# Performance work log

Hardware: AMD Instinct MI355X
Metric: run time of the kernel (lower is better)

The kernel has to match this reference:

```python
import jax, jax.numpy as jnp
import numpy as np

B, N, F = 4096, 128, 3
EPS = 1e-5


def _bn(x, g, b):
    # BatchNorm1d(element_num) on [B, N, C]: channels are dim 1 (the N elements);
    # training-mode stats over dims (0, 2), biased variance (torch default).
    m = x.mean(axis=(0, 2), keepdims=True)
    v = ((x - m) ** 2).mean(axis=(0, 2), keepdims=True)
    return (x - m) / jnp.sqrt(v + EPS) * g[None, :, None] + b[None, :, None]


def _rel(x, W, bvec, psi, phi, wr):
    # f'_i = wr/N * sum_{j != i} (psi*phi * <x_i, x_j>) * relu(unary(x_j))
    n = x.shape[1]
    U = jax.nn.relu(jnp.einsum('bnd,ed->bne', x, W) + bvec)       # [B,N,D]
    S = (psi * phi) * jnp.einsum('bnd,bmd->bnm', x, x)            # [B,N,N]
    S = S * (1.0 - jnp.eye(n, dtype=x.dtype))                     # exclude j == i
    return wr * jnp.einsum('bnm,bmd->bnd', S, U) / n


def setup_inputs() -> dict:
    key = jax.random.key(0)
    ks = iter(jax.random.split(key, 64))
    d1, d2 = 2 * F, 4 * F  # 6, 12

    def w(shape, s=0.1):
        return (jax.random.normal(next(ks), shape, dtype=jnp.float32) * s)

    def scalar():
        return jax.random.uniform(next(ks), (), dtype=jnp.float32)

    inp = {
        'x': jax.random.normal(next(ks), (B, N, F), dtype=jnp.float32),
        'fc1_w': w((d1, F)), 'fc1_b': w((d1,)),
        'bn1_g': jnp.ones((N,), jnp.float32), 'bn1_b': jnp.zeros((N,), jnp.float32),
        'fc2_w': w((d2, d1)), 'fc2_b': w((d2,)),
        'bn2_g': jnp.ones((N,), jnp.float32), 'bn2_b': jnp.zeros((N,), jnp.float32),
        'fc3_w': w((d2, d2)), 'fc3_b': w((d2,)),
        'u1_w': w((d2, d2)), 'u1_b': w((d2,)), 'ps1': scalar(), 'ph1': scalar(), 'wr1': scalar(),
        'u2_w': w((d2, d2)), 'u2_b': w((d2,)), 'ps2': scalar(), 'ph2': scalar(), 'wr2': scalar(),
        'u3_w': w((d2, d2)), 'u3_b': w((d2,)), 'ps3': scalar(), 'ph3': scalar(), 'wr3': scalar(),
        'u4_w': w((d2, d2)), 'u4_b': w((d2,)), 'ps4': scalar(), 'ph4': scalar(), 'wr4': scalar(),
        'fc4_w': w((d1, d2)), 'fc4_b': w((d1,)),
        'bn4_g': jnp.ones((N,), jnp.float32), 'bn4_b': jnp.zeros((N,), jnp.float32),
        'fc5_w': w((F, d1)), 'fc5_b': w((F,)),
        'fc6_w': w((1, F)), 'fc6_b': w((1,)),
        'fc7_w': w((F - 1, F)), 'fc7_b': w((F - 1,)),
        'fc8_w': w((1, F)), 'fc8_b': w((1,)),
    }
    return inp


def reference(x, fc1_w, fc1_b, bn1_g, bn1_b, fc2_w, fc2_b, bn2_g, bn2_b,
              fc3_w, fc3_b,
              u1_w, u1_b, ps1, ph1, wr1,
              u2_w, u2_b, ps2, ph2, wr2,
              u3_w, u3_b, ps3, ph3, wr3,
              u4_w, u4_b, ps4, ph4, wr4,
              fc4_w, fc4_b, bn4_g, bn4_b,
              fc5_w, fc5_b, fc6_w, fc6_b, fc7_w, fc7_b, fc8_w, fc8_b):
    h = jax.nn.relu(_bn(jnp.einsum('bnf,ef->bne', x, fc1_w) + fc1_b, bn1_g, bn1_b))
    h = jax.nn.relu(_bn(jnp.einsum('bnf,ef->bne', h, fc2_w) + fc2_b, bn2_g, bn2_b))
    h = jax.nn.sigmoid(jnp.einsum('bnf,ef->bne', h, fc3_w) + fc3_b)
    h = _rel(h, u1_w, u1_b, ps1, ph1, wr1)
    h = _rel(h, u2_w, u2_b, ps2, ph2, wr2)
    h = _rel(h, u3_w, u3_b, ps3, ph3, wr3)
    h = _rel(h, u4_w, u4_b, ps4, ph4, wr4)
    h = jax.nn.relu(_bn(jnp.einsum('bnf,ef->bne', h, fc4_w) + fc4_b, bn4_g, bn4_b))
    h = jax.nn.relu(jnp.einsum('bnf,ef->bne', h, fc5_w) + fc5_b)
    cls = jnp.einsum('bnf,ef->bne', h, fc6_w) + fc6_b          # [B,N,1]
    geo = jnp.einsum('bnf,ef->bne', h, fc7_w) + fc7_b          # [B,N,F-1]
    res = jnp.concatenate([cls, geo], axis=2)                   # [B,N,F]
    pres = res.max(axis=1)                                      # MaxPool1d over all N -> [B,F]
    pred = jax.nn.sigmoid(pres @ fc8_w.T + fc8_b)               # [B,1]
    return pred
```

## Files before the change

kernel.cpp:

```cpp
#include <hip/hip_runtime.h>
#include <hip/hip_fp16.h>

#define BB 4096
#define NN 128
#define EPS 1e-5f

#define S1 0
#define S2 2048
#define S4 4096
#define A4_OFF 6144

static __device__ __forceinline__ float sigmoidf_(float z){
  return 1.f/(1.f+__expf(-z));
}
static __device__ __forceinline__ float2 h2f2_(unsigned u){
  __half2 h = *reinterpret_cast<__half2*>(&u);
  return __half22float2(h);
}

static __device__ __forceinline__ float fdot2_(unsigned a, unsigned b, float c){
#if defined(__has_builtin)
#if __has_builtin(__builtin_amdgcn_fdot2)
  typedef _Float16 h2v __attribute__((ext_vector_type(2)));
  h2v av = *reinterpret_cast<h2v*>(&a);
  h2v bv = *reinterpret_cast<h2v*>(&b);
  return __builtin_amdgcn_fdot2(av, bv, c, false);
#else
  float2 af = h2f2_(a), bf = h2f2_(b);
  return fmaf(af.y, bf.y, fmaf(af.x, bf.x, c));
#endif
#else
  float2 af = h2f2_(a), bf = h2f2_(b);
  return fmaf(af.y, bf.y, fmaf(af.x, bf.x, c));
#endif
}

__global__ __launch_bounds__(256) void k1(const float* __restrict__ x, const float* __restrict__ w1,
                   const float* __restrict__ b1, float* __restrict__ st){
  __shared__ float bl[512];
  const int t = threadIdx.x;
  const int tid = blockIdx.x*256 + t;
  float W[18], Bv[6];
  #pragma unroll
  for (int i=0;i<18;i++) W[i]=w1[i];
  #pragma unroll
  for (int i=0;i<6;i++) Bv[i]=b1[i];
  float s=0.f, sq=0.f;
  #pragma unroll
  for (int kk=0;kk<2;kk++){
    const int r = tid + kk*262144;
    const float* xr = x + (size_t)r*3;
    float x0=xr[0], x1=xr[1], x2=xr[2];
    #pragma unroll
    for (int e=0;e<6;e++){
      float a = fmaf(x0,W[e*3+0], fmaf(x1,W[e*3+1], fmaf(x2,W[e*3+2], Bv[e])));
      s+=a; sq=fmaf(a,a,sq);
    }
  }
  bl[t]=s; bl[256+t]=sq;
  __syncthreads();
  const int shadow = (blockIdx.x & 7)*256;
  if (t<128) atomicAdd(&st[S1+shadow+t], bl[t]+bl[t+128]);
  else       atomicAdd(&st[S1+shadow+t], bl[t+128]+bl[t+256]);
}

__global__ __launch_bounds__(256) void k2(const float* __restrict__ x,
                   const float* __restrict__ w1, const float* __restrict__ b1,
                   const float* __restrict__ g1, const float* __restrict__ bb1,
                   const float* __restrict__ w2, const float* __restrict__ b2,
                   float* __restrict__ st){
  __shared__ float bl[512];
  const int t = threadIdx.x;
  const int tid = blockIdx.x*256 + t;
  const int n = t & 127;
  float ss=0.f, qs=0.f;
  #pragma unroll
  for (int c=0;c<8;c++){ ss+=st[S1+c*256+n]; qs+=st[S1+c*256+128+n]; }
  const float mean = ss*(1.f/(BB*6));
  const float var  = qs*(1.f/(BB*6)) - mean*mean;
  const float sc = g1[n]*rsqrtf(var+EPS), sh = bb1[n]-mean*sc;
  float W1[18], B1v[6], W2[72], B2v[12];
  #pragma unroll
  for (int i=0;i<18;i++) W1[i]=w1[i];
  #pragma unroll
  for (int i=0;i<6;i++) B1v[i]=b1[i];
  #pragma unroll
  for (int i=0;i<72;i++) W2[i]=w2[i];
  #pragma unroll
  for (int i=0;i<12;i++) B2v[i]=b2[i];
  float s=0.f, sq=0.f;
  #pragma unroll
  for (int kk=0;kk<2;kk++){
    const int r = tid + kk*262144;
    const float* xr = x + (size_t)r*3;
    float x0=xr[0], x1=xr[1], x2=xr[2];
    float h[6];
    #pragma unroll
    for (int e=0;e<6;e++){
      float a = fmaf(x0,W1[e*3+0], fmaf(x1,W1[e*3+1], fmaf(x2,W1[e*3+2], B1v[e])));
      h[e]=fmaxf(fmaf(a,sc,sh),0.f);
    }
    #pragma unroll
    for (int d=0;d<12;d++){
      float z=B2v[d];
      #pragma unroll
      for (int e=0;e<6;e++) z=fmaf(h[e],W2[d*6+e],z);
      s+=z; sq=fmaf(z,z,sq);
    }
  }
  bl[t]=s; bl[256+t]=sq;
  __syncthreads();
  const int shadow = (blockIdx.x & 7)*256;
  if (t<128) atomicAdd(&st[S2+shadow+t], bl[t]+bl[t+128]);
  else       atomicAdd(&st[S2+shadow+t], bl[t+128]+bl[t+256]);
}

__global__ __launch_bounds__(256) void k3(
  const float* __restrict__ x,
  const float* __restrict__ w1, const float* __restrict__ b1,
  const float* __restrict__ g1, const float* __restrict__ bb1,
  const float* __restrict__ w2, const float* __restrict__ b2,
  const float* __restrict__ g2, const float* __restrict__ bb2,
  const float* __restrict__ w3, const float* __restrict__ b3,
  const float* __restrict__ u1w, const float* __restrict__ u1b,
  const float* __restrict__ ps1, const float* __restrict__ ph1, const float* __restrict__ wr1,
  const float* __restrict__ u2w, const float* __restrict__ u2b,
  const float* __restrict__ ps2, const float* __restrict__ ph2, const float* __restrict__ wr2,
  const float* __restrict__ u3w, const float* __restrict__ u3b,
  const float* __restrict__ ps3, const float* __restrict__ ph3, const float* __restrict__ wr3,
  const float* __restrict__ u4w, const float* __restrict__ u4b,
  const float* __restrict__ ps4, const float* __restrict__ ph4, const float* __restrict__ wr4,
  const float* __restrict__ w4, const float* __restrict__ b4,
  __half* __restrict__ a4, float* __restrict__ st)
{
  __shared__ float lds[4][1536];
  const int wave = threadIdx.x >> 6;
  const int lane = threadIdx.x & 63;
  const int b = blockIdx.x*4 + wave;
  unsigned* Xp = (unsigned*)&lds[wave][0];
  unsigned* Up = (unsigned*)&lds[wave][768];
  const int r0 = lane*2, r1 = r0+1;

  float s1a=0,q1a=0,s1b=0,q1b=0,s2a=0,q2a=0,s2b=0,q2b=0;
  #pragma unroll
  for (int c=0;c<8;c++){
    s1a+=st[S1+c*256+r0]; q1a+=st[S1+c*256+128+r0];
    s1b+=st[S1+c*256+r1]; q1b+=st[S1+c*256+128+r1];
    s2a+=st[S2+c*256+r0]; q2a+=st[S2+c*256+128+r0];
    s2b+=st[S2+c*256+r1]; q2b+=st[S2+c*256+128+r1];
  }
  const float inv1 = 1.f/(BB*6), inv2 = 1.f/(BB*12);
  float m = s1a*inv1, v = q1a*inv1 - m*m;
  const float sA0 = g1[r0]*rsqrtf(v+EPS), hA0 = bb1[r0]-m*sA0;
  m = s1b*inv1; v = q1b*inv1 - m*m;
  const float sA1 = g1[r1]*rsqrtf(v+EPS), hA1 = bb1[r1]-m*sA1;
  m = s2a*inv2; v = q2a*inv2 - m*m;
  const float sB0 = g2[r0]*rsqrtf(v+EPS), hB0 = bb2[r0]-m*sB0;
  m = s2b*inv2; v = q2b*inv2 - m*m;
  const float sB1 = g2[r1]*rsqrtf(v+EPS), hB1 = bb2[r1]-m*sB1;

  const float2* xr = (const float2*)(x + ((size_t)b*128 + r0)*3);
  float2 c0=xr[0], c1=xr[1], c2=xr[2];
  const float xa0=c0.x, xa1=c0.y, xa2=c1.x;
  const float xb0=c1.y, xb1=c2.x, xb2=c2.y;

  float X0[12], X1[12];
  {
    float g6a[6], g6b[6];
    #pragma unroll
    for (int e=0;e<6;e++){
      float a0 = fmaf(xa0,w1[e*3+0], fmaf(xa1,w1[e*3+1], fmaf(xa2,w1[e*3+2], b1[e])));
      float a1v= fmaf(xb0,w1[e*3+0], fmaf(xb1,w1[e*3+1], fmaf(xb2,w1[e*3+2], b1[e])));
      g6a[e]=fmaxf(fmaf(a0,sA0,hA0),0.f);
      g6b[e]=fmaxf(fmaf(a1v,sA1,hA1),0.f);
    }
    float h0[12], h1[12];
    #pragma unroll
    for (int d=0;d<12;d++){
      float z0=b2[d], z1=b2[d];
      #pragma unroll
      for (int e=0;e<6;e++){ z0=fmaf(g6a[e],w2[d*6+e],z0); z1=fmaf(g6b[e],w2[d*6+e],z1); }
      h0[d]=fmaxf(fmaf(z0,sB0,hB0),0.f);
      h1[d]=fmaxf(fmaf(z1,sB1,hB1),0.f);
    }
    #pragma unroll
    for (int d=0; d<12; d++){
      float z0=b3[d], z1=b3[d];
      #pragma unroll
      for (int e=0;e<12;e++){ z0=fmaf(h0[e],w3[d*12+e],z0); z1=fmaf(h1[e],w3[d*12+e],z1); }
      X0[d]=sigmoidf_(z0); X1[d]=sigmoidf_(z1);
    }
  }

  const float* UW[4]  = {u1w,u2w,u3w,u4w};
  const float* UBv[4] = {u1b,u2b,u3b,u4b};
  const float cf[4] = {
    wr1[0]*ps1[0]*ph1[0]*(1.f/128.f),
    wr2[0]*ps2[0]*ph2[0]*(1.f/128.f),
    wr3[0]*ps3[0]*ph3[0]*(1.f/128.f),
    wr4[0]*ps4[0]*ph4[0]*(1.f/128.f)
  };

  const int g = lane>>4;
  int kc = lane & 15; if (kc>11) kc=11;

  #pragma unroll
  for (int l=0;l<4;l++){
    const float* uw = UW[l];
    const float* ub = UBv[l];
    const float coef = cf[l];
    float Y0[12], Y1[12];
    {
      float U0[12], U1[12];
      #pragma unroll
      for (int d=0;d<12;d++){
        float z0=ub[d], z1=ub[d];
        #pragma unroll
        for (int e=0;e<12;e++){ z0=fmaf(X0[e],uw[d*12+e],z0); z1=fmaf(X1[e],uw[d*12+e],z1); }
        U0[d]=fmaxf(z0,0.f); U1[d]=fmaxf(z1,0.f);
      }
      float q0=0.f, q1=0.f;
      #pragma unroll
      for (int e=0;e<12;e++){ q0=fmaf(X0[e],X0[e],q0); q1=fmaf(X1[e],X1[e],q1); }
      __half2 hp[12], up[12];
      #pragma unroll
      for (int e=0;e<12;e++){
        hp[e] = __floats2half2_rn(X0[e],X1[e]);
        up[e] = __floats2half2_rn(U0[e],U1[e]);
      }
      {
        const uint4* hpv = (const uint4*)hp;
        const uint4* upv = (const uint4*)up;
        uint4* xw = (uint4*)(Xp + lane*12);
        uint4* uwp = (uint4*)(Up + lane*12);
        xw[0]=hpv[0]; xw[1]=hpv[1]; xw[2]=hpv[2];
        uwp[0]=upv[0]; uwp[1]=upv[1]; uwp[2]=upv[2];
      }
      const float q0c = coef*q0, q1c = coef*q1;
      #pragma unroll
      for (int d=0;d<12;d++){ Y0[d] = -q0c*U0[d]; Y1[d] = -q1c*U1[d]; }
    }

    float mp[12];
    #pragma unroll
    for (int d=0;d<12;d++) mp[d]=0.f;
    #pragma unroll
    for (int i=0;i<16;i++){
      const int p = (g<<4) | ((i+g)&15);
      const unsigned xv2 = Xp[p*12 + kc];
      const uint4* urow = (const uint4*)(Up + p*12);
      uint4 ua=urow[0], ub4=urow[1], uc=urow[2];
      mp[0]=fdot2_(xv2, ua.x, mp[0]);  mp[1]=fdot2_(xv2, ua.y, mp[1]);
      mp[2]=fdot2_(xv2, ua.z, mp[2]);  mp[3]=fdot2_(xv2, ua.w, mp[3]);
      mp[4]=fdot2_(xv2, ub4.x, mp[4]); mp[5]=fdot2_(xv2, ub4.y, mp[5]);
      mp[6]=fdot2_(xv2, ub4.z, mp[6]); mp[7]=fdot2_(xv2, ub4.w, mp[7]);
      mp[8]=fdot2_(xv2, uc.x, mp[8]);  mp[9]=fdot2_(xv2, uc.y, mp[9]);
      mp[10]=fdot2_(xv2, uc.z, mp[10]); mp[11]=fdot2_(xv2, uc.w, mp[11]);
    }
    #pragma unroll
    for (int d=0;d<12;d++) mp[d] += __shfl_xor(mp[d], 16, 64);
    #pragma unroll
    for (int d=0;d<12;d++) mp[d] += __shfl_xor(mp[d], 32, 64);
    #pragma unroll
    for (int d=0;d<12;d++) mp[d] *= coef;

    #pragma unroll
    for (int k=0;k<12;k++){
      const float xa = X0[k], xb = X1[k];
      #pragma unroll
      for (int d=0;d<12;d++){
        const float mv = __int_as_float(__builtin_amdgcn_readlane(__float_as_int(mp[d]), k));
        Y0[d]=fmaf(xa,mv,Y0[d]); Y1[d]=fmaf(xb,mv,Y1[d]);
      }
    }
    #pragma unroll
    for (int d=0;d<12;d++){ X0[d]=Y0[d]; X1[d]=Y1[d]; }
  }

  float z0[6], z1[6];
  float s0=0.f,sq0=0.f,s1=0.f,sq1=0.f;
  #pragma unroll
  for (int e=0;e<6;e++){
    float a0=b4[e], a1v=b4[e];
    #pragma unroll
    for (int d=0;d<12;d++){ a0=fmaf(X0[d],w4[e*12+d],a0); a1v=fmaf(X1[d],w4[e*12+d],a1v); }
    z0[e]=a0; z1[e]=a1v;
    s0+=a0; sq0=fmaf(a0,a0,sq0); s1+=a1v; sq1=fmaf(a1v,a1v,sq1);
  }
  {
    __half2 ha[6];
    ha[0]=__floats2half2_rn(z0[0],z0[1]); ha[1]=__floats2half2_rn(z0[2],z0[3]); ha[2]=__floats2half2_rn(z0[4],z0[5]);
    ha[3]=__floats2half2_rn(z1[0],z1[1]); ha[4]=__floats2half2_rn(z1[2],z1[3]); ha[5]=__floats2half2_rn(z1[4],z1[5]);
    const uint2* hv = (const uint2*)ha;
    uint2* aw = (uint2*)(a4 + ((size_t)b*128 + r0)*6);
    aw[0]=hv[0]; aw[1]=hv[1]; aw[2]=hv[2];
  }

  __syncthreads();
  lds[wave][r0]=s0; lds[wave][r1]=s1;
  lds[wave][128+r0]=sq0; lds[wave][128+r1]=sq1;
  __syncthreads();
  const int t = threadIdx.x;
  const int c = (blockIdx.x & 7)*256;
  atomicAdd(&st[S4 + c + t], lds[0][t]+lds[1][t]+lds[2][t]+lds[3][t]);
}

__global__ __launch_bounds__(256) void k4(
  const __half* __restrict__ a4, const float* __restrict__ g4, const float* __restrict__ bb4,
  const float* __restrict__ w5, const float* __restrict__ b5,
  const float* __restrict__ w6, const float* __restrict__ b6,
  const float* __restrict__ w7, const float* __restrict__ b7,
  const float* __restrict__ w8, const float* __restrict__ b8,
  const float* __restrict__ st, float* __restrict__ out)
{
  const int wave = threadIdx.x>>6, lane = threadIdx.x&63;
  const int b = blockIdx.x*4 + wave;
  const int r0 = lane*2, r1 = r0+1;
  float ss0=0.f, qq0=0.f, ss1=0.f, qq1=0.f;
  #pragma unroll
  for (int cc=0;cc<8;cc++){
    ss0 += st[S4+cc*256+r0];     qq0 += st[S4+cc*256+128+r0];
    ss1 += st[S4+cc*256+r1];     qq1 += st[S4+cc*256+128+r1];
  }
  const float inv = 1.f/(BB*6);
  const float mean0 = ss0*inv, var0 = qq0*inv - mean0*mean0;
  const float sc0 = g4[r0]*rsqrtf(var0+EPS), sh0 = bb4[r0]-mean0*sc0;
  const float mean1 = ss1*inv, var1 = qq1*inv - mean1*mean1;
  const float sc1 = g4[r1]*rsqrtf(var1+EPS), sh1 = bb4[r1]-mean1*sc1;

  const uint2* ar = (const uint2*)(a4 + ((size_t)b*128 + r0)*6);
  uint2 v0=ar[0], v1=ar[1], v2=ar[2];
  float2 f0=h2f2_(v0.x), f1=h2f2_(v0.y), f2=h2f2_(v1.x);
  float2 f3=h2f2_(v1.y), f4=h2f2_(v2.x), f5=h2f2_(v2.y);
  float h0[6] = {f0.x,f0.y,f1.x,f1.y,f2.x,f2.y};
  float h1[6] = {f3.x,f3.y,f4.x,f4.y,f5.x,f5.y};
  #pragma unroll
  for (int e=0;e<6;e++){
    h0[e]=fmaxf(fmaf(h0[e],sc0,sh0),0.f);
    h1[e]=fmaxf(fmaf(h1[e],sc1,sh1),0.f);
  }
  float mx[3];
  {
    float h5a[3], h5b[3];
    #pragma unroll
    for (int f=0;f<3;f++){
      float za=b5[f], zb=b5[f];
      #pragma unroll
      for (int e=0;e<6;e++){ za=fmaf(h0[e],w5[f*6+e],za); zb=fmaf(h1[e],w5[f*6+e],zb); }
      h5a[f]=fmaxf(za,0.f); h5b[f]=fmaxf(zb,0.f);
    }
    float ca=b6[0], cb=b6[0];
    float g0a=b7[0], g0b=b7[0], g1a=b7[1], g1b=b7[1];
    #pragma unroll
    for (int f=0;f<3;f++){
      ca=fmaf(h5a[f],w6[f],ca);   cb=fmaf(h5b[f],w6[f],cb);
      g0a=fmaf(h5a[f],w7[f],g0a); g0b=fmaf(h5b[f],w7[f],g0b);
      g1a=fmaf(h5a[f],w7[3+f],g1a); g1b=fmaf(h5b[f],w7[3+f],g1b);
    }
    mx[0]=fmaxf(ca,cb); mx[1]=fmaxf(g0a,g0b); mx[2]=fmaxf(g1a,g1b);
  }
  #pragma unroll
  for (int off=32; off>0; off>>=1){
    mx[0]=fmaxf(mx[0], __shfl_xor(mx[0],off,64));
    mx[1]=fmaxf(mx[1], __shfl_xor(mx[1],off,64));
    mx[2]=fmaxf(mx[2], __shfl_xor(mx[2],off,64));
  }
  if (lane==0){
    float z = b8[0] + mx[0]*w8[0] + mx[1]*w8[1] + mx[2]*w8[2];
    out[b]=sigmoidf_(z);
  }
}

extern "C" void kernel_launch(void* const* d_in, const int* in_sizes, int n_in,
                              void* d_out, int out_size, void* d_ws, size_t ws_size,
                              hipStream_t stream){
  const float* x   = (const float*)d_in[0];
  const float* f1w = (const float*)d_in[1];
  const float* f1b = (const float*)d_in[2];
  const float* g1  = (const float*)d_in[3];
  const float* bb1 = (const float*)d_in[4];
  const float* f2w = (const float*)d_in[5];
  const float* f2b = (const float*)d_in[6];
  const float* g2  = (const float*)d_in[7];
  const float* bb2 = (const float*)d_in[8];
  const float* f3w = (const float*)d_in[9];
  const float* f3b = (const float*)d_in[10];
  const float* u1w = (const float*)d_in[11];
  const float* u1b = (const float*)d_in[12];
  const float* ps1 = (const float*)d_in[13];
  const float* ph1 = (const float*)d_in[14];
  const float* wr1 = (const float*)d_in[15];
  const float* u2w = (const float*)d_in[16];
  const float* u2b = (const float*)d_in[17];
  const float* ps2 = (const float*)d_in[18];
  const float* ph2 = (const float*)d_in[19];
  const float* wr2 = (const float*)d_in[20];
  const float* u3w = (const float*)d_in[21];
  const float* u3b = (const float*)d_in[22];
  const float* ps3 = (const float*)d_in[23];
  const float* ph3 = (const float*)d_in[24];
  const float* wr3 = (const float*)d_in[25];
  const float* u4w = (const float*)d_in[26];
  const float* u4b = (const float*)d_in[27];
  const float* ps4 = (const float*)d_in[28];
  const float* ph4 = (const float*)d_in[29];
  const float* wr4 = (const float*)d_in[30];
  const float* f4w = (const float*)d_in[31];
  const float* f4b = (const float*)d_in[32];
  const float* g4  = (const float*)d_in[33];
  const float* bb4 = (const float*)d_in[34];
  const float* f5w = (const float*)d_in[35];
  const float* f5b = (const float*)d_in[36];
  const float* f6w = (const float*)d_in[37];
  const float* f6b = (const float*)d_in[38];
  const float* f7w = (const float*)d_in[39];
  const float* f7b = (const float*)d_in[40];
  const float* f8w = (const float*)d_in[41];
  const float* f8b = (const float*)d_in[42];

  float* wsf = (float*)d_ws;
  float* st  = wsf;
  __half* a4 = (__half*)(wsf + A4_OFF);
  float* out = (float*)d_out;

  k1<<<dim3(1024), dim3(256), 0, stream>>>(x, f1w, f1b, st);
  k2<<<dim3(1024), dim3(256), 0, stream>>>(x, f1w, f1b, g1, bb1, f2w, f2b, st);
  k3<<<dim3(1024), dim3(256), 0, stream>>>(x, f1w, f1b, g1, bb1, f2w, f2b, g2, bb2,
      f3w, f3b,
      u1w,u1b,ps1,ph1,wr1, u2w,u2b,ps2,ph2,wr2,
      u3w,u3b,ps3,ph3,wr3, u4w,u4b,ps4,ph4,wr4,
      f4w, f4b, a4, st);
  k4<<<dim3(1024), dim3(256), 0, stream>>>(a4, g4, bb4, f5w, f5b,
      f6w, f6b, f7w, f7b, f8w, f8b, st, out);
}
```

Measured before the change: 199.9 us.

## Fuse four kernels into one persistent kernel with grid barriers between BatchNorm stages

Replaces the four separate launches with a single kernel that keeps per-row activations in registers across the BatchNorm statistic phases and uses a hierarchical atomic grid barrier to wait for the global sums. This removes recomputation of the early layers, the fp16 round-trip of the fc4 activations through global memory, and the launch gaps between kernels. It also switches arithmetic to two-wide float vectors for packed FMA. The design relies on all 1024 blocks being co-resident (launch bounds 256,4), adds a memset launch, and has a spin guard that could silently proceed if residency is not met.

```diff
diff --git a/kernel.cpp b/kernel.cpp
--- a/kernel.cpp
+++ b/kernel.cpp
@@ -8,7 +8,7 @@
 #define S1 0
 #define S2 2048
 #define S4 4096
-#define A4_OFF 6144
+#define BAR_OFF 6144
 
 static __device__ __forceinline__ float sigmoidf_(float z){
   return 1.f/(1.f+__expf(-z));
@@ -16,6 +16,35 @@
 static __device__ __forceinline__ float2 h2f2_(unsigned u){
   __half2 h = *reinterpret_cast<__half2*>(&u);
   return __half22float2(h);
+}
+
+typedef float v2f __attribute__((ext_vector_type(2)));
+static __device__ __forceinline__ v2f vfma(v2f a, v2f b, v2f c){
+#if defined(__has_builtin)
+#if __has_builtin(__builtin_elementwise_fma)
+  return __builtin_elementwise_fma(a,b,c);
+#else
+  v2f r; r.x=fmaf(a.x,b.x,c.x); r.y=fmaf(a.y,b.y,c.y); return r;
+#endif
+#else
+  v2f r; r.x=fmaf(a.x,b.x,c.x); r.y=fmaf(a.y,b.y,c.y); return r;
+#endif
+}
+static __device__ __forceinline__ v2f vfmas(v2f a, float s, v2f c){
+  v2f b = {s,s};
+  return vfma(a,b,c);
+}
+static __device__ __forceinline__ v2f vmax0(v2f a){
+#if defined(__has_builtin)
+#if __has_builtin(__builtin_elementwise_max)
+  v2f z = {0.f,0.f};
+  return __builtin_elementwise_max(a,z);
+#else
+  v2f r; r.x=fmaxf(a.x,0.f); r.y=fmaxf(a.y,0.f); return r;
+#endif
+#else
+  v2f r; r.x=fmaxf(a.x,0.f); r.y=fmaxf(a.y,0.f); return r;
+#endif
 }
 
 static __device__ __forceinline__ float fdot2_(unsigned a, unsigned b, float c){
@@ -35,87 +64,32 @@
 #endif
 }
 
-__global__ __launch_bounds__(256) void k1(const float* __restrict__ x, const float* __restrict__ w1,
-                   const float* __restrict__ b1, float* __restrict__ st){
-  __shared__ float bl[512];
-  const int t = threadIdx.x;
-  const int tid = blockIdx.x*256 + t;
-  float W[18], Bv[6];
-  #pragma unroll
-  for (int i=0;i<18;i++) W[i]=w1[i];
-  #pragma unroll
-  for (int i=0;i<6;i++) Bv[i]=b1[i];
-  float s=0.f, sq=0.f;
-  #pragma unroll
-  for (int kk=0;kk<2;kk++){
-    const int r = tid + kk*262144;
-    const float* xr = x + (size_t)r*3;
-    float x0=xr[0], x1=xr[1], x2=xr[2];
-    #pragma unroll
-    for (int e=0;e<6;e++){
-      float a = fmaf(x0,W[e*3+0], fmaf(x1,W[e*3+1], fmaf(x2,W[e*3+2], Bv[e])));
-      s+=a; sq=fmaf(a,a,sq);
-    }
-  }
-  bl[t]=s; bl[256+t]=sq;
+static __device__ __forceinline__ float cload_f(const float* p){
+  return __hip_atomic_load(p, __ATOMIC_RELAXED, __HIP_MEMORY_SCOPE_AGENT);
+}
+static __device__ __forceinline__ int cload_i(const int* p){
+  return __hip_atomic_load(p, __ATOMIC_RELAXED, __HIP_MEMORY_SCOPE_AGENT);
+}
+
+static __device__ __forceinline__ void gbar(int* __restrict__ bar, int phase){
   __syncthreads();
-  const int shadow = (blockIdx.x & 7)*256;
-  if (t<128) atomicAdd(&st[S1+shadow+t], bl[t]+bl[t+128]);
-  else       atomicAdd(&st[S1+shadow+t], bl[t+128]+bl[t+256]);
-}
-
-__global__ __launch_bounds__(256) void k2(const float* __restrict__ x,
-                   const float* __restrict__ w1, const float* __restrict__ b1,
-                   const float* __restrict__ g1, const float* __restrict__ bb1,
-                   const float* __restrict__ w2, const float* __restrict__ b2,
-                   float* __restrict__ st){
-  __shared__ float bl[512];
-  const int t = threadIdx.x;
-  const int tid = blockIdx.x*256 + t;
-  const int n = t & 127;
-  float ss=0.f, qs=0.f;
-  #pragma unroll
-  for (int c=0;c<8;c++){ ss+=st[S1+c*256+n]; qs+=st[S1+c*256+128+n]; }
-  const float mean = ss*(1.f/(BB*6));
-  const float var  = qs*(1.f/(BB*6)) - mean*mean;
-  const float sc = g1[n]*rsqrtf(var+EPS), sh = bb1[n]-mean*sc;
-  float W1[18], B1v[6], W2[72], B2v[12];
-  #pragma unroll
-  for (int i=0;i<18;i++) W1[i]=w1[i];
-  #pragma unroll
-  for (int i=0;i<6;i++) B1v[i]=b1[i];
-  #pragma unroll
-  for (int i=0;i<72;i++) W2[i]=w2[i];
-  #pragma unroll
-  for (int i=0;i<12;i++) B2v[i]=b2[i];
-  float s=0.f, sq=0.f;
-  #pragma unroll
-  for (int kk=0;kk<2;kk++){
-    const int r = tid + kk*262144;
-    const float* xr = x + (size_t)r*3;
-    float x0=xr[0], x1=xr[1], x2=xr[2];
-    float h[6];
-    #pragma unroll
-    for (int e=0;e<6;e++){
-      float a = fmaf(x0,W1[e*3+0], fmaf(x1,W1[e*3+1], fmaf(x2,W1[e*3+2], B1v[e])));
-      h[e]=fmaxf(fmaf(a,sc,sh),0.f);
-    }
-    #pragma unroll
-    for (int d=0;d<12;d++){
-      float z=B2v[d];
-      #pragma unroll
-      for (int e=0;e<6;e++) z=fmaf(h[e],W2[d*6+e],z);
-      s+=z; sq=fmaf(z,z,sq);
-    }
-  }
-  bl[t]=s; bl[256+t]=sq;
+  if (threadIdx.x == 0){
+    int* base = bar + phase*2048;
+    int* grp  = base + (blockIdx.x & 63)*16;
+    int* root = base + 1024;
+    int old = __hip_atomic_fetch_add(grp, 1, __ATOMIC_RELAXED, __HIP_MEMORY_SCOPE_AGENT);
+    if (old == 15)
+      __hip_atomic_fetch_add(root, 1, __ATOMIC_RELAXED, __HIP_MEMORY_SCOPE_AGENT);
+    int guard = 0;
+    while (cload_i(root) < 64 && guard < (1<<22)){
+      __builtin_amdgcn_s_sleep(1);
+      ++guard;
+    }
+  }
   __syncthreads();
-  const int shadow = (blockIdx.x & 7)*256;
-  if (t<128) atomicAdd(&st[S2+shadow+t], bl[t]+bl[t+128]);
-  else       atomicAdd(&st[S2+shadow+t], bl[t+128]+bl[t+256]);
-}
-
-__global__ __launch_bounds__(256) void k3(
+}
+
+__global__ __launch_bounds__(256, 4) void kf(
   const float* __restrict__ x,
   const float* __restrict__ w1, const float* __restrict__ b1,
   const float* __restrict__ g1, const float* __restrict__ bb1,
@@ -131,64 +105,107 @@
   const float* __restrict__ u4w, const float* __restrict__ u4b,
   const float* __restrict__ ps4, const float* __restrict__ ph4, const float* __restrict__ wr4,
   const float* __restrict__ w4, const float* __restrict__ b4,
-  __half* __restrict__ a4, float* __restrict__ st)
+  const float* __restrict__ g4, const float* __restrict__ bb4,
+  const float* __restrict__ w5, const float* __restrict__ b5,
+  const float* __restrict__ w6, const float* __restrict__ b6,
+  const float* __restrict__ w7, const float* __restrict__ b7,
+  const float* __restrict__ w8, const float* __restrict__ b8,
+  float* __restrict__ st, int* __restrict__ bar, float* __restrict__ out)
 {
   __shared__ float lds[4][1536];
-  const int wave = threadIdx.x >> 6;
-  const int lane = threadIdx.x & 63;
+  __shared__ float stg[256];
+  const int t = threadIdx.x;
+  const int wave = t >> 6, lane = t & 63;
   const int b = blockIdx.x*4 + wave;
+  const int r0 = lane*2, r1 = r0+1;
+  const int shadow = (blockIdx.x & 7)*256;
   unsigned* Xp = (unsigned*)&lds[wave][0];
   unsigned* Up = (unsigned*)&lds[wave][768];
-  const int r0 = lane*2, r1 = r0+1;
-
-  float s1a=0,q1a=0,s1b=0,q1b=0,s2a=0,q2a=0,s2b=0,q2b=0;
-  #pragma unroll
-  for (int c=0;c<8;c++){
-    s1a+=st[S1+c*256+r0]; q1a+=st[S1+c*256+128+r0];
-    s1b+=st[S1+c*256+r1]; q1b+=st[S1+c*256+128+r1];
-    s2a+=st[S2+c*256+r0]; q2a+=st[S2+c*256+128+r0];
-    s2b+=st[S2+c*256+r1]; q2b+=st[S2+c*256+128+r1];
-  }
-  const float inv1 = 1.f/(BB*6), inv2 = 1.f/(BB*12);
-  float m = s1a*inv1, v = q1a*inv1 - m*m;
-  const float sA0 = g1[r0]*rsqrtf(v+EPS), hA0 = bb1[r0]-m*sA0;
-  m = s1b*inv1; v = q1b*inv1 - m*m;
-  const float sA1 = g1[r1]*rsqrtf(v+EPS), hA1 = bb1[r1]-m*sA1;
-  m = s2a*inv2; v = q2a*inv2 - m*m;
-  const float sB0 = g2[r0]*rsqrtf(v+EPS), hB0 = bb2[r0]-m*sB0;
-  m = s2b*inv2; v = q2b*inv2 - m*m;
-  const float sB1 = g2[r1]*rsqrtf(v+EPS), hB1 = bb2[r1]-m*sB1;
 
   const float2* xr = (const float2*)(x + ((size_t)b*128 + r0)*3);
   float2 c0=xr[0], c1=xr[1], c2=xr[2];
-  const float xa0=c0.x, xa1=c0.y, xa2=c1.x;
-  const float xb0=c1.y, xb1=c2.x, xb2=c2.y;
-
-  float X0[12], X1[12];
+  const v2f xx0 = {c0.x, c1.y};
+  const v2f xx1 = {c0.y, c2.x};
+  const v2f xx2 = {c1.x, c2.y};
+
+  v2f a6[6];
   {
-    float g6a[6], g6b[6];
+    v2f s={0.f,0.f}, q={0.f,0.f};
     #pragma unroll
     for (int e=0;e<6;e++){
-      float a0 = fmaf(xa0,w1[e*3+0], fmaf(xa1,w1[e*3+1], fmaf(xa2,w1[e*3+2], b1[e])));
-      float a1v= fmaf(xb0,w1[e*3+0], fmaf(xb1,w1[e*3+1], fmaf(xb2,w1[e*3+2], b1[e])));
-      g6a[e]=fmaxf(fmaf(a0,sA0,hA0),0.f);
-      g6b[e]=fmaxf(fmaf(a1v,sA1,hA1),0.f);
-    }
-    float h0[12], h1[12];
+      v2f v = {b1[e], b1[e]};
+      v = vfmas(xx2, w1[e*3+2], v);
+      v = vfmas(xx1, w1[e*3+1], v);
+      v = vfmas(xx0, w1[e*3+0], v);
+      a6[e]=v;
+      s += v; q = vfma(v,v,q);
+    }
+    lds[wave][r0]=s.x; lds[wave][r1]=s.y;
+    lds[wave][128+r0]=q.x; lds[wave][128+r1]=q.y;
+    __syncthreads();
+    atomicAdd(&st[S1 + shadow + t], lds[0][t]+lds[1][t]+lds[2][t]+lds[3][t]);
+  }
+  gbar(bar, 0);
+
+  v2f zv[12];
+  {
+    float acc=0.f;
+    #pragma unroll
+    for (int c=0;c<8;c++) acc += cload_f(&st[S1 + c*256 + t]);
+    stg[t]=acc;
+    __syncthreads();
+    const float inv1 = 1.f/(BB*6);
+    float m=stg[r0]*inv1, v=stg[128+r0]*inv1-m*m;
+    const float sA0=g1[r0]*rsqrtf(v+EPS), hA0=bb1[r0]-m*sA0;
+    m=stg[r1]*inv1; v=stg[128+r1]*inv1-m*m;
+    const float sA1=g1[r1]*rsqrtf(v+EPS), hA1=bb1[r1]-m*sA1;
+    const v2f sA={sA0,sA1}, hA={hA0,hA1};
+
+    v2f h[6];
+    #pragma unroll
+    for (int e=0;e<6;e++) h[e]=vmax0(vfma(a6[e],sA,hA));
+
+    v2f s={0.f,0.f}, q={0.f,0.f};
     #pragma unroll
     for (int d=0;d<12;d++){
-      float z0=b2[d], z1=b2[d];
-      #pragma unroll
-      for (int e=0;e<6;e++){ z0=fmaf(g6a[e],w2[d*6+e],z0); z1=fmaf(g6b[e],w2[d*6+e],z1); }
-      h0[d]=fmaxf(fmaf(z0,sB0,hB0),0.f);
-      h1[d]=fmaxf(fmaf(z1,sB1,hB1),0.f);
-    }
-    #pragma unroll
-    for (int d=0; d<12; d++){
-      float z0=b3[d], z1=b3[d];
-      #pragma unroll
-      for (int e=0;e<12;e++){ z0=fmaf(h0[e],w3[d*12+e],z0); z1=fmaf(h1[e],w3[d*12+e],z1); }
-      X0[d]=sigmoidf_(z0); X1[d]=sigmoidf_(z1);
+      v2f z = {b2[d], b2[d]};
+      #pragma unroll
+      for (int e=0;e<6;e++) z = vfmas(h[e], w2[d*6+e], z);
+      zv[d]=z;
+      s += z; q = vfma(z,z,q);
+    }
+    __syncthreads();
+    lds[wave][r0]=s.x; lds[wave][r1]=s.y;
+    lds[wave][128+r0]=q.x; lds[wave][128+r1]=q.y;
+    __syncthreads();
+    atomicAdd(&st[S2 + shadow + t], lds[0][t]+lds[1][t]+lds[2][t]+lds[3][t]);
+  }
+  gbar(bar, 1);
+
+  v2f X[12];
+  {
+    float acc=0.f;
+    #pragma unroll
+    for (int c=0;c<8;c++) acc += cload_f(&st[S2 + c*256 + t]);
+    stg[t]=acc;
+    __syncthreads();
+    const float inv2 = 1.f/(BB*12);
+    float m=stg[r0]*inv2, v=stg[128+r0]*inv2-m*m;
+    const float sB0=g2[r0]*rsqrtf(v+EPS), hB0=bb2[r0]-m*sB0;
+    m=stg[r1]*inv2; v=stg[128+r1]*inv2-m*m;
+    const float sB1=g2[r1]*rsqrtf(v+EPS), hB1=bb2[r1]-m*sB1;
+    const v2f sB={sB0,sB1}, hB={hB0,hB1};
+
+    v2f h[12];
+    #pragma unroll
+    for (int d=0;d<12;d++) h[d]=vmax0(vfma(zv[d],sB,hB));
+    #pragma unroll
+    for (int d=0;d<12;d++){
+      v2f z = {b3[d], b3[d]};
+      #pragma unroll
+      for (int e=0;e<12;e++) z = vfmas(h[e], w3[d*12+e], z);
+      X[d].x = sigmoidf_(z.x);
+      X[d].y = sigmoidf_(z.y);
     }
   }
 
@@ -209,36 +226,36 @@
     const float* uw = UW[l];
     const float* ub = UBv[l];
     const float coef = cf[l];
-    float Y0[12], Y1[12];
+    v2f Y[12];
     {
-      float U0[12], U1[12];
+      v2f U[12];
       #pragma unroll
       for (int d=0;d<12;d++){
-        float z0=ub[d], z1=ub[d];
+        v2f z = {ub[d], ub[d]};
         #pragma unroll
-        for (int e=0;e<12;e++){ z0=fmaf(X0[e],uw[d*12+e],z0); z1=fmaf(X1[e],uw[d*12+e],z1); }
-        U0[d]=fmaxf(z0,0.f); U1[d]=fmaxf(z1,0.f);
-      }
-      float q0=0.f, q1=0.f;
-      #pragma unroll
-      for (int e=0;e<12;e++){ q0=fmaf(X0[e],X0[e],q0); q1=fmaf(X1[e],X1[e],q1); }
+        for (int e=0;e<12;e++) z = vfmas(X[e], uw[d*12+e], z);
+        U[d]=vmax0(z);
+      }
+      v2f q={0.f,0.f};
+      #pragma unroll
+      for (int e=0;e<12;e++) q = vfma(X[e],X[e],q);
       __half2 hp[12], up[12];
       #pragma unroll
       for (int e=0;e<12;e++){
-        hp[e] = __floats2half2_rn(X0[e],X1[e]);
-        up[e] = __floats2half2_rn(U0[e],U1[e]);
+        hp[e] = __floats2half2_rn(X[e].x, X[e].y);
+        up[e] = __floats2half2_rn(U[e].x, U[e].y);
       }
       {
         const uint4* hpv = (const uint4*)hp;
         const uint4* upv = (const uint4*)up;
-        uint4* xw = (uint4*)(Xp + lane*12);
+        uint4* xw  = (uint4*)(Xp + lane*12);
         uint4* uwp = (uint4*)(Up + lane*12);
         xw[0]=hpv[0]; xw[1]=hpv[1]; xw[2]=hpv[2];
         uwp[0]=upv[0]; uwp[1]=upv[1]; uwp[2]=upv[2];
       }
-      const float q0c = coef*q0, q1c = coef*q1;
-      #pragma unroll
-      for (int d=0;d<12;d++){ Y0[d] = -q0c*U0[d]; Y1[d] = -q1c*U1[d]; }
+      const v2f nqc = { -coef*q.x, -coef*q.y };
+      #pragma unroll
+      for (int d=0;d<12;d++) Y[d] = nqc * U[d];
     }
 
     float mp[12];
@@ -266,108 +283,83 @@
 
     #pragma unroll
     for (int k=0;k<12;k++){
-      const float xa = X0[k], xb = X1[k];
+      const v2f xk = X[k];
       #pragma unroll
       for (int d=0;d<12;d++){
         const float mv = __int_as_float(__builtin_amdgcn_readlane(__float_as_int(mp[d]), k));
-        Y0[d]=fmaf(xa,mv,Y0[d]); Y1[d]=fmaf(xb,mv,Y1[d]);
-      }
-    }
-    #pragma unroll
-    for (int d=0;d<12;d++){ X0[d]=Y0[d]; X1[d]=Y1[d]; }
-  }
-
-  float z0[6], z1[6];
-  float s0=0.f,sq0=0.f,s1=0.f,sq1=0.f;
-  #pragma unroll
-  for (int e=0;e<6;e++){
-    float a0=b4[e], a1v=b4[e];
-    #pragma unroll
-    for (int d=0;d<12;d++){ a0=fmaf(X0[d],w4[e*12+d],a0); a1v=fmaf(X1[d],w4[e*12+d],a1v); }
-    z0[e]=a0; z1[e]=a1v;
-    s0+=a0; sq0=fmaf(a0,a0,sq0); s1+=a1v; sq1=fmaf(a1v,a1v,sq1);
-  }
+        Y[d] = vfmas(xk, mv, Y[d]);
+      }
+    }
+    #pragma unroll
+    for (int d=0;d<12;d++) X[d]=Y[d];
+  }
+
+  v2f z4[6];
   {
-    __half2 ha[6];
-    ha[0]=__floats2half2_rn(z0[0],z0[1]); ha[1]=__floats2half2_rn(z0[2],z0[3]); ha[2]=__floats2half2_rn(z0[4],z0[5]);
-    ha[3]=__floats2half2_rn(z1[0],z1[1]); ha[4]=__floats2half2_rn(z1[2],z1[3]); ha[5]=__floats2half2_rn(z1[4],z1[5]);
-    const uint2* hv = (const uint2*)ha;
-    uint2* aw = (uint2*)(a4 + ((size_t)b*128 + r0)*6);
-    aw[0]=hv[0]; aw[1]=hv[1]; aw[2]=hv[2];
-  }
-
-  __syncthreads();
-  lds[wave][r0]=s0; lds[wave][r1]=s1;
-  lds[wave][128+r0]=sq0; lds[wave][128+r1]=sq1;
-  __syncthreads();
-  const int t = threadIdx.x;
-  const int c = (blockIdx.x & 7)*256;
-  atomicAdd(&st[S4 + c + t], lds[0][t]+lds[1][t]+lds[2][t]+lds[3][t]);
-}
-
-__global__ __launch_bounds__(256) void k4(
-  const __half* __restrict__ a4, const float* __restrict__ g4, const float* __restrict__ bb4,
-  const float* __restrict__ w5, const float* __restrict__ b5,
-  const float* __restrict__ w6, const float* __restrict__ b6,
-  const float* __restrict__ w7, const float* __restrict__ b7,
-  const float* __restrict__ w8, const float* __restrict__ b8,
-  const float* __restrict__ st, float* __restrict__ out)
-{
-  const int wave = threadIdx.x>>6, lane = threadIdx.x&63;
-  const int b = blockIdx.x*4 + wave;
-  const int r0 = lane*2, r1 = r0+1;
-  float ss0=0.f, qq0=0.f, ss1=0.f, qq1=0.f;
-  #pragma unroll
-  for (int cc=0;cc<8;cc++){
-    ss0 += st[S4+cc*256+r0];     qq0 += st[S4+cc*256+128+r0];
-    ss1 += st[S4+cc*256+r1];     qq1 += st[S4+cc*256+128+r1];
-  }
-  const float inv = 1.f/(BB*6);
-  const float mean0 = ss0*inv, var0 = qq0*inv - mean0*mean0;
-  const float sc0 = g4[r0]*rsqrtf(var0+EPS), sh0 = bb4[r0]-mean0*sc0;
-  const float mean1 = ss1*inv, var1 = qq1*inv - mean1*mean1;
-  const float sc1 = g4[r1]*rsqrtf(var1+EPS), sh1 = bb4[r1]-mean1*sc1;
-
-  const uint2* ar = (const uint2*)(a4 + ((size_t)b*128 + r0)*6);
-  uint2 v0=ar[0], v1=ar[1], v2=ar[2];
-  float2 f0=h2f2_(v0.x), f1=h2f2_(v0.y), f2=h2f2_(v1.x);
-  float2 f3=h2f2_(v1.y), f4=h2f2_(v2.x), f5=h2f2_(v2.y);
-  float h0[6] = {f0.x,f0.y,f1.x,f1.y,f2.x,f2.y};
-  float h1[6] = {f3.x,f3.y,f4.x,f4.y,f5.x,f5.y};
-  #pragma unroll
-  for (int e=0;e<6;e++){
-    h0[e]=fmaxf(fmaf(h0[e],sc0,sh0),0.f);
-    h1[e]=fmaxf(fmaf(h1[e],sc1,sh1),0.f);
-  }
-  float mx[3];
+    v2f s={0.f,0.f}, q={0.f,0.f};
+    #pragma unroll
+    for (int e=0;e<6;e++){
+      v2f a = {b4[e], b4[e]};
+      #pragma unroll
+      for (int d=0;d<12;d++) a = vfmas(X[d], w4[e*12+d], a);
+      z4[e]=a;
+      s += a; q = vfma(a,a,q);
+    }
+    __syncthreads();
+    lds[wave][r0]=s.x; lds[wave][r1]=s.y;
+    lds[wave][128+r0]=q.x; lds[wave][128+r1]=q.y;
+    __syncthreads();
+    atomicAdd(&st[S4 + shadow + t], lds[0][t]+lds[1][t]+lds[2][t]+lds[3][t]);
+  }
+  gbar(bar, 2);
+
   {
-    float h5a[3], h5b[3];
-    #pragma unroll
-    for (int f=0;f<3;f++){
-      float za=b5[f], zb=b5[f];
-      #pragma unroll
-      for (int e=0;e<6;e++){ za=fmaf(h0[e],w5[f*6+e],za); zb=fmaf(h1[e],w5[f*6+e],zb); }
-      h5a[f]=fmaxf(za,0.f); h5b[f]=fmaxf(zb,0.f);
-    }
-    float ca=b6[0], cb=b6[0];
-    float g0a=b7[0], g0b=b7[0], g1a=b7[1], g1b=b7[1];
-    #pragma unroll
-    for (int f=0;f<3;f++){
-      ca=fmaf(h5a[f],w6[f],ca);   cb=fmaf(h5b[f],w6[f],cb);
-      g0a=fmaf(h5a[f],w7[f],g0a); g0b=fmaf(h5b[f],w7[f],g0b);
-      g1a=fmaf(h5a[f],w7[3+f],g1a); g1b=fmaf(h5b[f],w7[3+f],g1b);
-    }
-    mx[0]=fmaxf(ca,cb); mx[1]=fmaxf(g0a,g0b); mx[2]=fmaxf(g1a,g1b);
-  }
-  #pragma unroll
-  for (int off=32; off>0; off>>=1){
-    mx[0]=fmaxf(mx[0], __shfl_xor(mx[0],off,64));
-    mx[1]=fmaxf(mx[1], __shfl_xor(mx[1],off,64));
-    mx[2]=fmaxf(mx[2], __shfl_xor(mx[2],off,64));
-  }
-  if (lane==0){
-    float z = b8[0] + mx[0]*w8[0] + mx[1]*w8[1] + mx[2]*w8[2];
-    out[b]=sigmoidf_(z);
+    float acc=0.f;
+    #pragma unroll
+    for (int c=0;c<8;c++) acc += cload_f(&st[S4 + c*256 + t]);
+    stg[t]=acc;
+    __syncthreads();
+    const float inv = 1.f/(BB*6);
+    const float mean0=stg[r0]*inv, var0=stg[128+r0]*inv-mean0*mean0;
+    const float sc0=g4[r0]*rsqrtf(var0+EPS), sh0=bb4[r0]-mean0*sc0;
+    const float mean1=stg[r1]*inv, var1=stg[128+r1]*inv-mean1*mean1;
+    const float sc1=g4[r1]*rsqrtf(var1+EPS), sh1=bb4[r1]-mean1*sc1;
+    const v2f sc={sc0,sc1}, sh={sh0,sh1};
+
+    v2f h[6];
+    #pragma unroll
+    for (int e=0;e<6;e++) h[e]=vmax0(vfma(z4[e],sc,sh));
+
+    float mx[3];
+    {
+      v2f h5[3];
+      #pragma unroll
+      for (int f=0;f<3;f++){
+        v2f z = {b5[f], b5[f]};
+        #pragma unroll
+        for (int e=0;e<6;e++) z = vfmas(h[e], w5[f*6+e], z);
+        h5[f]=vmax0(z);
+      }
+      v2f ca = {b6[0], b6[0]};
+      v2f g0 = {b7[0], b7[0]}, g1v = {b7[1], b7[1]};
+      #pragma unroll
+      for (int f=0;f<3;f++){
+        ca  = vfmas(h5[f], w6[f],   ca);
+        g0  = vfmas(h5[f], w7[f],   g0);
+        g1v = vfmas(h5[f], w7[3+f], g1v);
+      }
+      mx[0]=fmaxf(ca.x,ca.y); mx[1]=fmaxf(g0.x,g0.y); mx[2]=fmaxf(g1v.x,g1v.y);
+    }
+    #pragma unroll
+    for (int off=32; off>0; off>>=1){
+      mx[0]=fmaxf(mx[0], __shfl_xor(mx[0],off,64));
+      mx[1]=fmaxf(mx[1], __shfl_xor(mx[1],off,64));
+      mx[2]=fmaxf(mx[2], __shfl_xor(mx[2],off,64));
+    }
+    if (lane==0){
+      float z = b8[0] + mx[0]*w8[0] + mx[1]*w8[1] + mx[2]*w8[2];
+      out[b]=sigmoidf_(z);
+    }
   }
 }
 
@@ -420,16 +412,22 @@
 
   float* wsf = (float*)d_ws;
   float* st  = wsf;
-  __half* a4 = (__half*)(wsf + A4_OFF);
+  int*   bar = (int*)(wsf + BAR_OFF);
   float* out = (float*)d_out;
 
-  k1<<<dim3(1024), dim3(256), 0, stream>>>(x, f1w, f1b, st);
-  k2<<<dim3(1024), dim3(256), 0, stream>>>(x, f1w, f1b, g1, bb1, f2w, f2b, st);
-  k3<<<dim3(1024), dim3(256), 0, stream>>>(x, f1w, f1b, g1, bb1, f2w, f2b, g2, bb2,
+  hipMemsetAsync(bar, 0, 3*2048*sizeof(int), stream);
+
+  kf<<<dim3(1024), dim3(256), 0, stream>>>(
+      x,
+      f1w, f1b, g1, bb1,
+      f2w, f2b, g2, bb2,
       f3w, f3b,
-      u1w,u1b,ps1,ph1,wr1, u2w,u2b,ps2,ph2,wr2,
-      u3w,u3b,ps3,ph3,wr3, u4w,u4b,ps4,ph4,wr4,
-      f4w, f4b, a4, st);
-  k4<<<dim3(1024), dim3(256), 0, stream>>>(a4, g4, bb4, f5w, f5b,
-      f6w, f6b, f7w, f7b, f8w, f8b, st, out);
-}
+      u1w, u1b, ps1, ph1, wr1,
+      u2w, u2b, ps2, ph2, wr2,
+      u3w, u3b, ps3, ph3, wr3,
+      u4w, u4b, ps4, ph4, wr4,
+      f4w, f4b, g4, bb4,
+      f5w, f5b, f6w, f6b,
+      f7w, f7b, f8w, f8b,
+      st, bar, out);
+}
```

Measured after the change: 206.0 us. 3.1% more time.
